# Kernel tuning notes

Hardware: AMD Instinct MI355X
Metric: run time of the kernel (lower is better)

## Reference

```python
import jax, jax.numpy as jnp
import numpy as np

NUM_WIRES = 512
BATCH = 65536
HBAR = 2.0  # PennyLane default.gaussian convention; sqrt(2*hbar) = 2


def setup_inputs() -> dict:
    key = jax.random.key(0)
    ks = jax.random.split(key, 8)
    state_batch = jax.random.normal(ks[0], (BATCH, NUM_WIRES), dtype=jnp.float32)
    squeeze = jax.random.normal(ks[1], (NUM_WIRES,), dtype=jnp.float32)
    phase = jax.random.normal(ks[2], (NUM_WIRES,), dtype=jnp.float32)
    disp = jax.random.normal(ks[3], (NUM_WIRES,), dtype=jnp.float32)
    squeeze2 = jax.random.normal(ks[4], (NUM_WIRES,), dtype=jnp.float32)
    kerr = jax.random.normal(ks[5], (NUM_WIRES,), dtype=jnp.float32)
    head_w = jax.random.normal(ks[6], (1, NUM_WIRES), dtype=jnp.float32) / np.sqrt(NUM_WIRES)
    head_b = jnp.zeros((1,), dtype=jnp.float32)
    return {
        "state_batch": state_batch,
        "squeeze": squeeze,
        "phase": phase,
        "disp": disp,
        "squeeze2": squeeze2,
        "kerr": kerr,
        "head_w": head_w,
        "head_b": head_b,
    }


def _cv_features(x, squeeze, phase, disp, squeeze2):
    # Gaussian-state mean propagation per wire, vacuum start, hbar=2.
    # S(r,0): xbar *= e^-r ; R(phi): xbar' = xbar*cos(phi) (pbar=0 before rotation)
    # D(d,0): xbar += 2d ; S(r2,0): xbar *= e^-r2
    # Kerr is non-Gaussian: identity on the Gaussian mean vector (unsupported on
    # default.gaussian; omitted from the quadrature-mean evolution).
    # expval(X) = xbar
    root2h = np.sqrt(2.0 * HBAR)  # = 2
    return jnp.exp(-squeeze2) * (root2h * x * jnp.exp(-squeeze) * jnp.cos(phase) + root2h * disp)


def reference(state_batch, squeeze, phase, disp, squeeze2, kerr, head_w, head_b):
    x = state_batch[:, :NUM_WIRES]  # torch.real of a real tensor is identity
    feats = _cv_features(x, squeeze, phase, disp, squeeze2)  # [B, W]
    out = feats @ head_w.T + head_b  # [B, 1]
    return out.squeeze(-1)
```

## Files before the change

### kernel.cpp

```cpp
#include <hip/hip_runtime.h>
#include <hip/hip_bf16.h>
#include <math.h>

#define NUM_WIRES 512
#define BATCH 65536

__global__ void prep_kernel(const float* __restrict__ squeeze,
                            const float* __restrict__ phase,
                            const float* __restrict__ disp,
                            const float* __restrict__ squeeze2,
                            const float* __restrict__ head_w,
                            const float* __restrict__ head_b,
                            float* __restrict__ coeff_bias) {
    const int j = threadIdx.x;
    const float root2h = 2.0f;
    float e2 = __expf(-squeeze2[j]);
    e2 = expf(-squeeze2[j]);
    const float a = root2h * e2 * expf(-squeeze[j]) * cosf(phase[j]);
    const float w = head_w[j];
    coeff_bias[j] = w * a;

    __shared__ float red[NUM_WIRES];
    red[j] = w * root2h * e2 * disp[j];
    __syncthreads();
    for (int s = NUM_WIRES / 2; s > 0; s >>= 1) {
        if (j < s) red[j] += red[j + s];
        __syncthreads();
    }
    if (j == 0) coeff_bias[NUM_WIRES] = red[0] + head_b[0];
}

__global__ __launch_bounds__(256) void dot_kernel(const float* __restrict__ x,
                                                  const float* __restrict__ coeff_bias,
                                                  float* __restrict__ out,
                                                  int rows) {
    const int lane = threadIdx.x & 63;
    const int waveInBlock = threadIdx.x >> 6;
    const int wavesPerBlock = blockDim.x >> 6;
    const int waveStride = gridDim.x * wavesPerBlock;

    const float4 c0 = *reinterpret_cast<const float4*>(coeff_bias + lane * 4);
    const float4 c1 = *reinterpret_cast<const float4*>(coeff_bias + 256 + lane * 4);
    const float bias = coeff_bias[NUM_WIRES];

    for (int row = blockIdx.x * wavesPerBlock + waveInBlock; row < rows; row += waveStride) {
        const float4* p = reinterpret_cast<const float4*>(x + (size_t)row * NUM_WIRES);
        const float4 a = p[lane];
        const float4 b = p[64 + lane];
        float s = a.x * c0.x + a.y * c0.y + a.z * c0.z + a.w * c0.w
                + b.x * c1.x + b.y * c1.y + b.z * c1.z + b.w * c1.w;
        #pragma unroll
        for (int off = 32; off >= 1; off >>= 1)
            s += __shfl_xor(s, off, 64);
        if (lane == 0) out[row] = s + bias;
    }
}

extern "C" void kernel_launch(void* const* d_in, const int* in_sizes, int n_in,
                              void* d_out, int out_size, void* d_ws, size_t ws_size,
                              hipStream_t stream) {
    const float* state_batch = (const float*)d_in[0];
    const float* squeeze     = (const float*)d_in[1];
    const float* phase       = (const float*)d_in[2];
    const float* disp        = (const float*)d_in[3];
    const float* squeeze2    = (const float*)d_in[4];
    const float* head_w      = (const float*)d_in[6];
    const float* head_b      = (const float*)d_in[7];
    float* out = (float*)d_out;
    float* coeff_bias = (float*)d_ws;

    prep_kernel<<<1, NUM_WIRES, 0, stream>>>(squeeze, phase, disp, squeeze2,
                                             head_w, head_b, coeff_bias);
    dot_kernel<<<2048, 256, 0, stream>>>(state_batch, coeff_bias, out, out_size);
}
```

Measured before the change: 30.55 us.

## Fuse coefficient prep into dot kernel and process two rows per iteration

Removes the separate single-block prep kernel and has every block recompute the 512 folded coefficients and the bias into shared memory before doing the row dot products. Each wave now handles 8 fixed rows, two at a time, with interleaved loads and shuffle reductions to raise memory-level parallelism. This removes one launch and the serial dependency between the two kernels, at the cost of redundant per-block transcendental math and a block-wide reduction before any row loads start.

```diff
diff --git a/kernel.cpp b/kernel.cpp
--- a/kernel.cpp
+++ b/kernel.cpp
@@ -3,56 +3,66 @@
 #include <math.h>
 
 #define NUM_WIRES 512
-#define BATCH 65536
 
-__global__ void prep_kernel(const float* __restrict__ squeeze,
-                            const float* __restrict__ phase,
-                            const float* __restrict__ disp,
-                            const float* __restrict__ squeeze2,
-                            const float* __restrict__ head_w,
-                            const float* __restrict__ head_b,
-                            float* __restrict__ coeff_bias) {
-    const int j = threadIdx.x;
-    const float root2h = 2.0f;
-    float e2 = __expf(-squeeze2[j]);
-    e2 = expf(-squeeze2[j]);
-    const float a = root2h * e2 * expf(-squeeze[j]) * cosf(phase[j]);
-    const float w = head_w[j];
-    coeff_bias[j] = w * a;
+__global__ __launch_bounds__(256, 8) void fused_dot_kernel(
+        const float* __restrict__ x,
+        const float* __restrict__ squeeze,
+        const float* __restrict__ phase,
+        const float* __restrict__ disp,
+        const float* __restrict__ squeeze2,
+        const float* __restrict__ head_w,
+        const float* __restrict__ head_b,
+        float* __restrict__ out, int rows) {
+    __shared__ float s_coeff[NUM_WIRES];
+    __shared__ float s_red[256];
 
-    __shared__ float red[NUM_WIRES];
-    red[j] = w * root2h * e2 * disp[j];
+    const int t = threadIdx.x;
+    float partial = 0.0f;
+    #pragma unroll
+    for (int k = 0; k < 2; ++k) {
+        const int j = t + k * 256;
+        const float e2 = expf(-squeeze2[j]);
+        const float w  = head_w[j];
+        s_coeff[j] = w * 2.0f * e2 * expf(-squeeze[j]) * cosf(phase[j]);
+        partial += w * 2.0f * e2 * disp[j];
+    }
+    s_red[t] = partial;
     __syncthreads();
-    for (int s = NUM_WIRES / 2; s > 0; s >>= 1) {
-        if (j < s) red[j] += red[j + s];
+    #pragma unroll
+    for (int s = 128; s > 0; s >>= 1) {
+        if (t < s) s_red[t] += s_red[t + s];
         __syncthreads();
     }
-    if (j == 0) coeff_bias[NUM_WIRES] = red[0] + head_b[0];
-}
+    const float bias = s_red[0] + head_b[0];
 
-__global__ __launch_bounds__(256) void dot_kernel(const float* __restrict__ x,
-                                                  const float* __restrict__ coeff_bias,
-                                                  float* __restrict__ out,
-                                                  int rows) {
-    const int lane = threadIdx.x & 63;
-    const int waveInBlock = threadIdx.x >> 6;
-    const int wavesPerBlock = blockDim.x >> 6;
-    const int waveStride = gridDim.x * wavesPerBlock;
+    const int lane = t & 63;
+    const int wave = t >> 6;
+    const float4 c0 = *reinterpret_cast<const float4*>(&s_coeff[lane * 4]);
+    const float4 c1 = *reinterpret_cast<const float4*>(&s_coeff[256 + lane * 4]);
 
-    const float4 c0 = *reinterpret_cast<const float4*>(coeff_bias + lane * 4);
-    const float4 c1 = *reinterpret_cast<const float4*>(coeff_bias + 256 + lane * 4);
-    const float bias = coeff_bias[NUM_WIRES];
-
-    for (int row = blockIdx.x * wavesPerBlock + waveInBlock; row < rows; row += waveStride) {
-        const float4* p = reinterpret_cast<const float4*>(x + (size_t)row * NUM_WIRES);
-        const float4 a = p[lane];
-        const float4 b = p[64 + lane];
-        float s = a.x * c0.x + a.y * c0.y + a.z * c0.z + a.w * c0.w
-                + b.x * c1.x + b.y * c1.y + b.z * c1.z + b.w * c1.w;
+    const int waveId = blockIdx.x * 4 + wave;
+    const int base = waveId * 8;
+    #pragma unroll
+    for (int i = 0; i < 4; ++i) {
+        const int r0 = base + 2 * i;
+        if (r0 + 1 >= rows + 1) break;
+        const float4* p0 = reinterpret_cast<const float4*>(x + (size_t)r0 * NUM_WIRES);
+        const float4* p1 = reinterpret_cast<const float4*>(x + (size_t)(r0 + 1) * NUM_WIRES);
+        const float4 a0 = p0[lane];
+        const float4 b0 = p0[64 + lane];
+        const float4 a1 = p1[lane];
+        const float4 b1 = p1[64 + lane];
+        float s0 = a0.x * c0.x + a0.y * c0.y + a0.z * c0.z + a0.w * c0.w
+                 + b0.x * c1.x + b0.y * c1.y + b0.z * c1.z + b0.w * c1.w;
+        float s1 = a1.x * c0.x + a1.y * c0.y + a1.z * c0.z + a1.w * c0.w
+                 + b1.x * c1.x + b1.y * c1.y + b1.z * c1.z + b1.w * c1.w;
         #pragma unroll
-        for (int off = 32; off >= 1; off >>= 1)
-            s += __shfl_xor(s, off, 64);
-        if (lane == 0) out[row] = s + bias;
+        for (int off = 32; off >= 1; off >>= 1) {
+            s0 += __shfl_xor(s0, off, 64);
+            s1 += __shfl_xor(s1, off, 64);
+        }
+        if (lane == 0) out[r0] = s0 + bias;
+        if (lane == 1 && r0 + 1 < rows) out[r0 + 1] = s1 + bias;
     }
 }
 
@@ -67,9 +77,7 @@
     const float* head_w      = (const float*)d_in[6];
     const float* head_b      = (const float*)d_in[7];
     float* out = (float*)d_out;
-    float* coeff_bias = (float*)d_ws;
 
-    prep_kernel<<<1, NUM_WIRES, 0, stream>>>(squeeze, phase, disp, squeeze2,
-                                             head_w, head_b, coeff_bias);
-    dot_kernel<<<2048, 256, 0, stream>>>(state_batch, coeff_bias, out, out_size);
+    fused_dot_kernel<<<2048, 256, 0, stream>>>(state_batch, squeeze, phase, disp,
+                                               squeeze2, head_w, head_b, out, out_size);
 }
```

New measurement: 26.76 us. 12.4% less time.
